# Performance work log

Hardware: AMD Instinct MI355X
Metric: run time of the kernel (lower is better)

## Reference

```python
import jax, jax.numpy as jnp
import numpy as np

N_NODES = 100000
N_EDGES = 1600000
FEAT = 128
EMB = 32
N_GRAPHS = 512


def gcn_conv(x, W, b, src, dst, deg_inv_sqrt):
    # PyG GCNConv: h = x @ W; propagate with norm = d_i^{-1/2} d_j^{-1/2} over A + I
    h = x @ W  # [N, out]
    norm = deg_inv_sqrt[src] * deg_inv_sqrt[dst]  # [E]
    msg = h[src] * norm[:, None]  # gather + scale
    agg = jax.ops.segment_sum(msg, dst, num_segments=N_NODES)
    # self-loop contribution: norm_ii = d_i^{-1}
    agg = agg + h * (deg_inv_sqrt * deg_inv_sqrt)[:, None]
    return agg + b


def setup_inputs() -> dict:
    key = jax.random.key(0)
    ks = jax.random.split(key, 10)
    x = jax.random.normal(ks[0], (N_NODES, FEAT), dtype=jnp.float32)
    edge_index = jax.random.randint(ks[1], (2, N_EDGES), 0, N_NODES, dtype=jnp.int64)
    batch_index = jnp.sort(jax.random.randint(ks[2], (N_NODES,), 0, N_GRAPHS, dtype=jnp.int64))
    # Glorot-ish init for weights (PyG GCNConv lin has no bias arg here but conv bias exists)
    def glorot(k, fan_in, fan_out):
        s = jnp.sqrt(6.0 / (fan_in + fan_out)).astype(jnp.float32)
        return jax.random.uniform(k, (fan_in, fan_out), jnp.float32, -s, s)
    W1 = glorot(ks[3], FEAT, EMB)
    b1 = jnp.zeros((EMB,), jnp.float32)
    W2 = glorot(ks[4], EMB, EMB)
    b2 = jnp.zeros((EMB,), jnp.float32)
    Wo = glorot(ks[5], EMB, 1)
    bo = jnp.zeros((1,), jnp.float32)
    return {"x": x, "edge_index": edge_index, "batch_index": batch_index,
            "W1": W1, "b1": b1, "W2": W2, "b2": b2, "Wo": Wo, "bo": bo}


def reference(x, edge_index, batch_index, W1, b1, W2, b2, Wo, bo):
    src, dst = edge_index[0], edge_index[1]
    # degree over A + I (edge weights = 1, counted on dst as in PyG)
    deg = jax.ops.segment_sum(jnp.ones((N_EDGES,), x.dtype), dst, num_segments=N_NODES) + 1.0
    deg_inv_sqrt = jax.lax.rsqrt(deg)

    out = jax.nn.relu(gcn_conv(x, W1, b1, src, dst, deg_inv_sqrt))
    out = jax.nn.relu(gcn_conv(out, W2, b2, src, dst, deg_inv_sqrt))

    # global mean pool over graphs
    summed = jax.ops.segment_sum(out, batch_index, num_segments=N_GRAPHS)  # [G, EMB]
    counts = jax.ops.segment_sum(jnp.ones((N_NODES,), x.dtype), batch_index, num_segments=N_GRAPHS)
    pooled = summed / jnp.maximum(counts, 1.0)[:, None]

    return pooled @ Wo + bo  # [G, 1]
```

## Files before the change

kernel.cpp:

```cpp
#include <hip/hip_runtime.h>
#include <hip/hip_fp16.h>

#define N_NODES 100000
#define N_EDGES 1600000
#define N_GRAPHS 512
#define FEAT 128
#define EMB 32
#define ZROW N_NODES
#define PADCAP (N_EDGES + 8 * N_NODES)
#define NCOPY 64
#define NBKT 250
#define NPB 400
#define ABLK 1024
#define EPB 1563
#define NTILE (N_NODES / 16)
#define AGB (N_NODES / 32)

typedef unsigned short u16;
typedef unsigned int u32;
typedef _Float16 f16;
typedef float f32x4 __attribute__((ext_vector_type(4)));
typedef unsigned short u16x4 __attribute__((ext_vector_type(4)));
typedef f16 f16x8 __attribute__((ext_vector_type(8)));

__device__ __forceinline__ int pad8(int d) { return (d + 7) & ~7; }

__device__ __forceinline__ float4 h4_to_f4(u16x4 v) {
  union { unsigned int u; __half2 h; } a, b;
  a.u = (unsigned int)v.x | ((unsigned int)v.y << 16);
  b.u = (unsigned int)v.z | ((unsigned int)v.w << 16);
  float2 f0 = __half22float2(a.h);
  float2 f1 = __half22float2(b.h);
  return make_float4(f0.x, f0.y, f1.x, f1.y);
}

__device__ __forceinline__ u16x4 f4_to_h4(float4 f) {
  union { unsigned int u; __half2 h; } a, b;
  a.h = __float22half2_rn(make_float2(f.x, f.y));
  b.h = __float22half2_rn(make_float2(f.z, f.w));
  u16x4 r;
  r.x = (u16)(a.u & 0xffff); r.y = (u16)(a.u >> 16);
  r.z = (u16)(b.u & 0xffff); r.w = (u16)(b.u >> 16);
  return r;
}


__global__ __launch_bounds__(256) void k_node_init(const int* __restrict__ degcnt,
                                                   float* __restrict__ dis,
                                                   u16* __restrict__ hs1) {
  int i = blockIdx.x * 256 + threadIdx.x;
  if (i < N_NODES) dis[i] = rsqrtf((float)degcnt[i] + 1.0f);
  if (i < EMB) hs1[(size_t)ZROW * EMB + i] = 0;
}

__global__ __launch_bounds__(512) void k_gcnt(const int* __restrict__ batch,
                                              int* __restrict__ gcnt) {
  __shared__ int first[N_GRAPHS + 1];
  int g = threadIdx.x;
  int lo = 0, hi = N_NODES;
  while (lo < hi) {
    int mid = (lo + hi) >> 1;
    if (batch[mid] < g) lo = mid + 1; else hi = mid;
  }
  first[g] = lo;
  if (g == 0) first[N_GRAPHS] = N_NODES;
  __syncthreads();
  gcnt[g] = first[g + 1] - first[g];
}


__global__ __launch_bounds__(256) void k_scanA(const int* __restrict__ degcnt,
                                               int* __restrict__ blocksum) {
  __shared__ int sh[256];
  int t = threadIdx.x;
  int base = blockIdx.x * 1024;
  int s = 0;
#pragma unroll
  for (int j = 0; j < 4; j++) {
    int idx = base + t * 4 + j;
    if (idx < N_NODES) s += pad8(degcnt[idx]);
  }
  sh[t] = s;
  __syncthreads();
  for (int off = 128; off > 0; off >>= 1) {
    if (t < off) sh[t] += sh[t + off];
    __syncthreads();
  }
  if (t == 0) blocksum[blockIdx.x] = sh[0];
}

__global__ __launch_bounds__(128) void k_scanB(const int* __restrict__ blocksum,
                                               int* __restrict__ blockoff,
                                               int* __restrict__ total_out, int nb) {
  __shared__ int sh[128];
  int t = threadIdx.x;
  int v = (t < nb) ? blocksum[t] : 0;
  sh[t] = v;
  __syncthreads();
  for (int off = 1; off < 128; off <<= 1) {
    int add = (t >= off) ? sh[t - off] : 0;
    __syncthreads();
    sh[t] += add;
    __syncthreads();
  }
  if (t < nb) blockoff[t] = sh[t] - v;
  if (t == nb - 1) total_out[0] = sh[t];
}

__global__ __launch_bounds__(256) void k_scanC(const int* __restrict__ degcnt,
                                               const int* __restrict__ blockoff,
                                               int* __restrict__ row_ptr) {
  __shared__ int sh[256];
  int t = threadIdx.x;
  int base = blockIdx.x * 1024;
  int v[4];
#pragma unroll
  for (int j = 0; j < 4; j++) {
    int idx = base + t * 4 + j;
    v[j] = (idx < N_NODES) ? pad8(degcnt[idx]) : 0;
  }
  int tsum = v[0] + v[1] + v[2] + v[3];
  sh[t] = tsum;
  __syncthreads();
  for (int off = 1; off < 256; off <<= 1) {
    int add = (t >= off) ? sh[t - off] : 0;
    __syncthreads();
    sh[t] += add;
    __syncthreads();
  }
  int p = sh[t] - tsum + blockoff[blockIdx.x];
#pragma unroll
  for (int j = 0; j < 4; j++) {
    int idx = base + t * 4 + j;
    if (idx < N_NODES) row_ptr[idx] = p;
    p += v[j];
  }
}


__global__ __launch_bounds__(256) void k_binA(const int* __restrict__ dst,
                                              int* __restrict__ cnt) {
  __shared__ int h[NBKT];
  int k = blockIdx.x, t = threadIdx.x;
  for (int i = t; i < NBKT; i += 256) h[i] = 0;
  __syncthreads();
  int e0 = k * EPB;
  int e1 = min(e0 + EPB, N_EDGES);
  for (int e = e0 + t; e < e1; e += 256)
    atomicAdd(&h[(u32)dst[e] / (u32)NPB], 1);
  __syncthreads();
  for (int i = t; i < NBKT; i += 256) cnt[k * NBKT + i] = h[i];
}

__global__ __launch_bounds__(256) void k_binscanA(const int* __restrict__ cnt,
                                                  int* __restrict__ off,
                                                  int* __restrict__ tot) {
  __shared__ int sh[256];
  int b = blockIdx.x, t = threadIdx.x;
  int v[4];
#pragma unroll
  for (int j = 0; j < 4; j++) v[j] = cnt[(t * 4 + j) * NBKT + b];
  int tsum = v[0] + v[1] + v[2] + v[3];
  sh[t] = tsum;
  __syncthreads();
  for (int o = 1; o < 256; o <<= 1) {
    int add = (t >= o) ? sh[t - o] : 0;
    __syncthreads();
    sh[t] += add;
    __syncthreads();
  }
  int p = sh[t] - tsum;
#pragma unroll
  for (int j = 0; j < 4; j++) {
    off[(t * 4 + j) * NBKT + b] = p;
    p += v[j];
  }
  if (t == 255) tot[b] = p;
}

__global__ __launch_bounds__(256) void k_binscanB(const int* __restrict__ tot,
                                                  int* __restrict__ base) {
  __shared__ int sh[256];
  int t = threadIdx.x;
  int v = (t < NBKT) ? tot[t] : 0;
  sh[t] = v;
  __syncthreads();
  for (int o = 1; o < 256; o <<= 1) {
    int add = (t >= o) ? sh[t - o] : 0;
    __syncthreads();
    sh[t] += add;
    __syncthreads();
  }
  if (t < NBKT) base[t] = sh[t] - v;
  if (t == NBKT - 1) base[NBKT] = sh[t];
}

__global__ __launch_bounds__(256) void k_binscat(const int* __restrict__ src,
                                                 const int* __restrict__ dst,
                                                 const int* __restrict__ off,
                                                 const int* __restrict__ base,
                                                 u32* __restrict__ binbuf) {
  __shared__ int posB[NBKT];
  __shared__ int h[NBKT];
  int k = blockIdx.x, t = threadIdx.x;
  for (int i = t; i < NBKT; i += 256) {
    posB[i] = base[i] + off[k * NBKT + i];
    h[i] = 0;
  }
  __syncthreads();
  int e0 = k * EPB;
  int e1 = min(e0 + EPB, N_EDGES);
  for (int e = e0 + t; e < e1; e += 256) {
    u32 d = (u32)dst[e];
    int b = d / (u32)NPB;
    int r = atomicAdd(&h[b], 1);
    binbuf[posB[b] + r] = (u32)src[e] * (u32)NPB + (d - (u32)b * NPB);
  }
}

__global__ __launch_bounds__(256) void k_bdeg(const u32* __restrict__ binbuf,
                                              const int* __restrict__ base,
                                              int* __restrict__ degcnt) {
  __shared__ int c[NPB];
  int b = blockIdx.x, t = threadIdx.x;
  for (int i = t; i < NPB; i += 256) c[i] = 0;
  __syncthreads();
  int s0 = base[b], s1 = base[b + 1];
  for (int i = s0 + t; i < s1; i += 256) {
    u32 p = binbuf[i];
    u32 s = p / (u32)NPB;
    atomicAdd(&c[p - s * (u32)NPB], 1);
  }
  __syncthreads();
  for (int i = t; i < NPB; i += 256) degcnt[b * NPB + i] = c[i];
}

__global__ __launch_bounds__(256) void k_fillB(const u32* __restrict__ binbuf,
                                               const int* __restrict__ base,
                                               const int* __restrict__ row_ptr,
                                               int* __restrict__ col) {
  __shared__ int rp[NPB + 1];
  __shared__ int cur[NPB];
  int b = blockIdx.x, t = threadIdx.x;
  for (int i = t; i < NPB + 1; i += 256) rp[i] = row_ptr[b * NPB + i];
  for (int i = t; i < NPB; i += 256) cur[i] = 0;
  __syncthreads();
  int s0 = base[b], s1 = base[b + 1];
  for (int i = s0 + t; i < s1; i += 256) {
    u32 p = binbuf[i];
    u32 s = p / (u32)NPB;
    int ld = p - s * (u32)NPB;
    int pos = atomicAdd(&cur[ld], 1);
    col[rp[ld] + pos] = (int)s;
  }
  __syncthreads();
  for (int ld = t; ld < NPB; ld += 256) {
    int bs = rp[ld], len = rp[ld + 1] - bs, c = cur[ld];
    for (int j = c; j < len; j++) col[bs + j] = ZROW;
  }
}


__global__ __launch_bounds__(256) void k_gemm1(const float* __restrict__ x,
                                               const float* __restrict__ W1,
                                               const float* __restrict__ dis,
                                               u16* __restrict__ hs1) {
  int wid = (blockIdx.x * 256 + threadIdx.x) >> 6;
  if (wid >= NTILE) return;
  int l = threadIdx.x & 63;
  int m = l & 15, q = l >> 4;
  f16x8 B[4][2];
#pragma unroll
  for (int s = 0; s < 4; ++s)
#pragma unroll
    for (int h = 0; h < 2; ++h)
#pragma unroll
      for (int j = 0; j < 8; ++j)
        B[s][h][j] = (f16)W1[(s * 32 + q * 8 + j) * EMB + h * 16 + m];
  int row = wid * 16 + m;
  const float* xr = x + (size_t)row * FEAT + q * 8;
  f32x4 acc0 = {0.f, 0.f, 0.f, 0.f}, acc1 = {0.f, 0.f, 0.f, 0.f};
#pragma unroll
  for (int s = 0; s < 4; ++s) {
    f32x4 xa = __builtin_nontemporal_load((const f32x4*)(xr + s * 32));
    f32x4 xb = __builtin_nontemporal_load((const f32x4*)(xr + s * 32 + 4));
    f16x8 A;
    A[0] = (f16)xa.x; A[1] = (f16)xa.y; A[2] = (f16)xa.z; A[3] = (f16)xa.w;
    A[4] = (f16)xb.x; A[5] = (f16)xb.y; A[6] = (f16)xb.z; A[7] = (f16)xb.w;
    acc0 = __builtin_amdgcn_mfma_f32_16x16x32_f16(A, B[s][0], acc0, 0, 0, 0);
    acc1 = __builtin_amdgcn_mfma_f32_16x16x32_f16(A, B[s][1], acc1, 0, 0, 0);
  }
  f32x4 dq = *(const f32x4*)(dis + wid * 16 + q * 4);
  u16* o = hs1 + (size_t)(wid * 16) * EMB;
#pragma unroll
  for (int i = 0; i < 4; ++i) {
    int r = q * 4 + i;
    float dv = (i == 0) ? dq.x : (i == 1) ? dq.y : (i == 2) ? dq.z : dq.w;
    o[(size_t)r * EMB + m]      = __half_as_ushort(__float2half_rn(acc0[i] * dv));
    o[(size_t)r * EMB + 16 + m] = __half_as_ushort(__float2half_rn(acc1[i] * dv));
  }
}

__global__ __launch_bounds__(256) void k_gemm2(const u16* __restrict__ in1,
                                               const float* __restrict__ W2,
                                               const float* __restrict__ dis,
                                               u16* __restrict__ hs2) {
  int wid = (blockIdx.x * 256 + threadIdx.x) >> 6;
  if (wid >= NTILE) return;
  int l = threadIdx.x & 63;
  int m = l & 15, q = l >> 4;
  f16x8 B[2];
#pragma unroll
  for (int h = 0; h < 2; ++h)
#pragma unroll
    for (int j = 0; j < 8; ++j)
      B[h][j] = (f16)W2[(q * 8 + j) * EMB + h * 16 + m];
  int row = wid * 16 + m;
  f16x8 A = *(const f16x8*)(in1 + (size_t)row * EMB + q * 8);
  f32x4 acc0 = {0.f, 0.f, 0.f, 0.f}, acc1 = {0.f, 0.f, 0.f, 0.f};
  acc0 = __builtin_amdgcn_mfma_f32_16x16x32_f16(A, B[0], acc0, 0, 0, 0);
  acc1 = __builtin_amdgcn_mfma_f32_16x16x32_f16(A, B[1], acc1, 0, 0, 0);
  f32x4 dq = *(const f32x4*)(dis + wid * 16 + q * 4);
  u16* o = hs2 + (size_t)(wid * 16) * EMB;
#pragma unroll
  for (int i = 0; i < 4; ++i) {
    int r = q * 4 + i;
    float dv = (i == 0) ? dq.x : (i == 1) ? dq.y : (i == 2) ? dq.z : dq.w;
    o[(size_t)r * EMB + m]      = __half_as_ushort(__float2half_rn(acc0[i] * dv));
    o[(size_t)r * EMB + 16 + m] = __half_as_ushort(__float2half_rn(acc1[i] * dv));
  }
}


__device__ __forceinline__ void acc4(float4& A, u16x4 v) {
  float4 f = h4_to_f4(v);
  A.x += f.x; A.y += f.y; A.z += f.z; A.w += f.w;
}

__device__ __forceinline__ float4 agg_node(const u16* __restrict__ hs,
                                           const int* __restrict__ row_ptr,
                                           const int* __restrict__ col,
                                           int node, int sub) {
  const u16x4* t4 = (const u16x4*)hs;
  int a0 = row_ptr[node];
  int na = row_ptr[node + 1] - a0;
  const int* cp = col + a0;
  int4 c0 = *(const int4*)cp;
  int4 c1 = *(const int4*)(cp + 4);
  float4 A = make_float4(0.f, 0.f, 0.f, 0.f);
  for (int i = 0; i < na; i += 8) {
    u16x4 v0 = t4[(size_t)c0.x * 8 + sub];
    u16x4 v1 = t4[(size_t)c0.y * 8 + sub];
    u16x4 v2 = t4[(size_t)c0.z * 8 + sub];
    u16x4 v3 = t4[(size_t)c0.w * 8 + sub];
    u16x4 v4 = t4[(size_t)c1.x * 8 + sub];
    u16x4 v5 = t4[(size_t)c1.y * 8 + sub];
    u16x4 v6 = t4[(size_t)c1.z * 8 + sub];
    u16x4 v7 = t4[(size_t)c1.w * 8 + sub];
    if (i + 8 < na) {
      c0 = *(const int4*)(cp + i + 8);
      c1 = *(const int4*)(cp + i + 12);
    }
    acc4(A, v0); acc4(A, v1); acc4(A, v2); acc4(A, v3);
    acc4(A, v4); acc4(A, v5); acc4(A, v6); acc4(A, v7);
  }
  acc4(A, t4[(size_t)node * 8 + sub]);
  return A;
}

__device__ __forceinline__ float4 relu_row(float4 acc, float d, float4 bq) {
  float4 o;
  o.x = fmaxf(fmaf(acc.x, d, bq.x), 0.f);
  o.y = fmaxf(fmaf(acc.y, d, bq.y), 0.f);
  o.z = fmaxf(fmaf(acc.z, d, bq.z), 0.f);
  o.w = fmaxf(fmaf(acc.w, d, bq.w), 0.f);
  return o;
}

__global__ __launch_bounds__(256) void k_agg1(const u16* __restrict__ hs,
                                              const int* __restrict__ row_ptr,
                                              const int* __restrict__ col,
                                              const float* __restrict__ dis,
                                              const float* __restrict__ b,
                                              u16* __restrict__ out) {
  int t = threadIdx.x;
  int l = t & 63;
  int node = blockIdx.x * 32 + (t >> 6) * 8 + (l >> 3);
  int sub = l & 7;
  float4 A = agg_node(hs, row_ptr, col, node, sub);
  float4 bq = ((const float4*)b)[sub];
  float4 o = relu_row(A, dis[node], bq);
  ((u16x4*)(out + (size_t)node * EMB))[sub] = f4_to_h4(o);
}

__global__ __launch_bounds__(256) void k_agg2pool(const u16* __restrict__ hs,
                                                  const int* __restrict__ row_ptr,
                                                  const int* __restrict__ col,
                                                  const float* __restrict__ dis,
                                                  const float* __restrict__ b2,
                                                  const float* __restrict__ Wo,
                                                  const int* __restrict__ batch,
                                                  float* __restrict__ gaccP) {
  int t = threadIdx.x;
  int l = t & 63;
  int node = blockIdx.x * 32 + (t >> 6) * 8 + (l >> 3);
  int sub = l & 7;
  float4 A = agg_node(hs, row_ptr, col, node, sub);
  float4 bq = ((const float4*)b2)[sub];
  float4 wq = ((const float4*)Wo)[sub];
  float4 o = relu_row(A, dis[node], bq);
  float p = o.x * wq.x + o.y * wq.y + o.z * wq.z + o.w * wq.w;
  p += __shfl_xor(p, 1);
  p += __shfl_xor(p, 2);
  p += __shfl_xor(p, 4);
  if (sub == 0)
    atomicAdd(&gaccP[(node & (NCOPY - 1)) * N_GRAPHS + batch[node]], p);
}

__global__ __launch_bounds__(256) void k_finalize(const float* __restrict__ gaccP,
                                                  const int* __restrict__ gcnt,
                                                  const float* __restrict__ bo,
                                                  float* __restrict__ out) {
  int g = blockIdx.x * 256 + threadIdx.x;
  if (g < N_GRAPHS) {
    float s = 0.f;
#pragma unroll 8
    for (int c = 0; c < NCOPY; ++c) s += gaccP[c * N_GRAPHS + g];
    out[g] = s / fmaxf((float)gcnt[g], 1.0f) + bo[0];
  }
}


extern "C" void kernel_launch(void* const* d_in, const int* in_sizes, int n_in,
                              void* d_out, int out_size, void* d_ws, size_t ws_size,
                              hipStream_t stream) {
  const float* x     = (const float*)d_in[0];
  const int*   ei    = (const int*)d_in[1];
  const int*   batch = (const int*)d_in[2];
  const float* W1    = (const float*)d_in[3];
  const float* b1    = (const float*)d_in[4];
  const float* W2    = (const float*)d_in[5];
  const float* b2    = (const float*)d_in[6];
  const float* Wo    = (const float*)d_in[7];
  const float* bo    = (const float*)d_in[8];
  float* out = (float*)d_out;

  const int* src = ei;
  const int* dst = ei + N_EDGES;

  char* w = (char*)d_ws;
  float* gaccP   = (float*)w;  w += (size_t)NCOPY * N_GRAPHS * 4;
  size_t zero_bytes = (size_t)(w - (char*)d_ws);
  int*   degcnt  = (int*)w;    w += (size_t)N_NODES * 4;
  int*   gcnt    = (int*)w;    w += (size_t)N_GRAPHS * 4;
  int*   row_ptr = (int*)w;    w += (size_t)(N_NODES + 4) * 4;
  int*   blocksum= (int*)w;    w += 128 * 4;
  int*   blockoff= (int*)w;    w += 128 * 4;
  int*   cnt     = (int*)w;    w += (size_t)ABLK * NBKT * 4;
  int*   boff    = (int*)w;    w += (size_t)ABLK * NBKT * 4;
  int*   btot    = (int*)w;    w += (size_t)(NBKT + 8) * 4;
  int*   bbase   = (int*)w;    w += (size_t)(NBKT + 8) * 4;
  int*   col     = (int*)w;    w += (size_t)PADCAP * 4;
  float* dis     = (float*)w;  w += (size_t)N_NODES * 4;
  u16*   hs1     = (u16*)w;    w += (size_t)(N_NODES + 1) * EMB * 2;
  u16*   out1    = (u16*)w;    w += (size_t)N_NODES * EMB * 2;
  u32*   binbuf  = (u32*)out1;
  u16*   hs2     = hs1;

  const int NB  = (N_NODES + 255) / 256;
  const int SB  = (N_NODES + 1023) / 1024;
  const int GB  = (NTILE * 64 + 255) / 256;

  (void)hipMemsetAsync(d_ws, 0, zero_bytes, stream);

  k_binA<<<ABLK, 256, 0, stream>>>(dst, cnt);
  k_binscanA<<<NBKT, 256, 0, stream>>>(cnt, boff, btot);
  k_binscanB<<<1, 256, 0, stream>>>(btot, bbase);
  k_binscat<<<ABLK, 256, 0, stream>>>(src, dst, boff, bbase, binbuf);
  k_bdeg<<<NBKT, 256, 0, stream>>>(binbuf, bbase, degcnt);

  k_node_init<<<NB, 256, 0, stream>>>(degcnt, dis, hs1);
  k_gcnt<<<1, 512, 0, stream>>>(batch, gcnt);
  k_scanA<<<SB, 256, 0, stream>>>(degcnt, blocksum);
  k_scanB<<<1, 128, 0, stream>>>(blocksum, blockoff, row_ptr + N_NODES, SB);
  k_scanC<<<SB, 256, 0, stream>>>(degcnt, blockoff, row_ptr);
  k_fillB<<<NBKT, 256, 0, stream>>>(binbuf, bbase, row_ptr, col);

  k_gemm1<<<GB, 256, 0, stream>>>(x, W1, dis, hs1);
  k_agg1<<<AGB, 256, 0, stream>>>(hs1, row_ptr, col, dis, b1, out1);
  k_gemm2<<<GB, 256, 0, stream>>>(out1, W2, dis, hs2);
  k_agg2pool<<<AGB, 256, 0, stream>>>(hs2, row_ptr, col, dis, b2, Wo, batch, gaccP);
  k_finalize<<<2, 256, 0, stream>>>(gaccP, gcnt, bo, out);
}
```

Measured before the change: 247.1 us.

## Drop CSR build; aggregate directly from dst-binned edge buffer via LDS atomics

Removes the CSR construction (degree scan kernels, fill kernel, padded col array) and instead aggregates neighbor features straight from the dst-bucketed edge buffer. Each block owns a 100-node bucket and accumulates messages into a shared-memory float accumulator with LDS atomics, then applies self-loop, normalization, bias and ReLU. Degree and rsqrt are fused into one kernel, and bucket counts and block sizes are retuned. This saves several launches and the col write and read, at the cost of LDS atomic contention and unordered float summation.

```diff
diff --git a/kernel.cpp b/kernel.cpp
--- a/kernel.cpp
+++ b/kernel.cpp
@@ -7,14 +7,14 @@
 #define FEAT 128
 #define EMB 32
 #define ZROW N_NODES
-#define PADCAP (N_EDGES + 8 * N_NODES)
 #define NCOPY 64
-#define NBKT 250
-#define NPB 400
-#define ABLK 1024
-#define EPB 1563
+#define NBKT 1000
+#define NPB 100
+#define LDSW 33
+#define ABLK 512
+#define EPB 3125
 #define NTILE (N_NODES / 16)
-#define AGB (N_NODES / 32)
+#define SENT ((u32)ZROW * (u32)NPB)
 
 typedef unsigned short u16;
 typedef unsigned int u32;
@@ -22,8 +22,6 @@
 typedef float f32x4 __attribute__((ext_vector_type(4)));
 typedef unsigned short u16x4 __attribute__((ext_vector_type(4)));
 typedef f16 f16x8 __attribute__((ext_vector_type(8)));
-
-__device__ __forceinline__ int pad8(int d) { return (d + 7) & ~7; }
 
 __device__ __forceinline__ float4 h4_to_f4(u16x4 v) {
   union { unsigned int u; __half2 h; } a, b;
@@ -44,14 +42,15 @@
   return r;
 }
 
-
-__global__ __launch_bounds__(256) void k_node_init(const int* __restrict__ degcnt,
-                                                   float* __restrict__ dis,
-                                                   u16* __restrict__ hs1) {
-  int i = blockIdx.x * 256 + threadIdx.x;
-  if (i < N_NODES) dis[i] = rsqrtf((float)degcnt[i] + 1.0f);
-  if (i < EMB) hs1[(size_t)ZROW * EMB + i] = 0;
-}
+__device__ __forceinline__ float4 relu_row(float4 acc, float d, float4 bq) {
+  float4 o;
+  o.x = fmaxf(fmaf(acc.x, d, bq.x), 0.f);
+  o.y = fmaxf(fmaf(acc.y, d, bq.y), 0.f);
+  o.z = fmaxf(fmaf(acc.z, d, bq.z), 0.f);
+  o.w = fmaxf(fmaf(acc.w, d, bq.w), 0.f);
+  return o;
+}
+
 
 __global__ __launch_bounds__(512) void k_gcnt(const int* __restrict__ batch,
                                               int* __restrict__ gcnt) {
@@ -69,75 +68,6 @@
 }
 
 
-__global__ __launch_bounds__(256) void k_scanA(const int* __restrict__ degcnt,
-                                               int* __restrict__ blocksum) {
-  __shared__ int sh[256];
-  int t = threadIdx.x;
-  int base = blockIdx.x * 1024;
-  int s = 0;
-#pragma unroll
-  for (int j = 0; j < 4; j++) {
-    int idx = base + t * 4 + j;
-    if (idx < N_NODES) s += pad8(degcnt[idx]);
-  }
-  sh[t] = s;
-  __syncthreads();
-  for (int off = 128; off > 0; off >>= 1) {
-    if (t < off) sh[t] += sh[t + off];
-    __syncthreads();
-  }
-  if (t == 0) blocksum[blockIdx.x] = sh[0];
-}
-
-__global__ __launch_bounds__(128) void k_scanB(const int* __restrict__ blocksum,
-                                               int* __restrict__ blockoff,
-                                               int* __restrict__ total_out, int nb) {
-  __shared__ int sh[128];
-  int t = threadIdx.x;
-  int v = (t < nb) ? blocksum[t] : 0;
-  sh[t] = v;
-  __syncthreads();
-  for (int off = 1; off < 128; off <<= 1) {
-    int add = (t >= off) ? sh[t - off] : 0;
-    __syncthreads();
-    sh[t] += add;
-    __syncthreads();
-  }
-  if (t < nb) blockoff[t] = sh[t] - v;
-  if (t == nb - 1) total_out[0] = sh[t];
-}
-
-__global__ __launch_bounds__(256) void k_scanC(const int* __restrict__ degcnt,
-                                               const int* __restrict__ blockoff,
-                                               int* __restrict__ row_ptr) {
-  __shared__ int sh[256];
-  int t = threadIdx.x;
-  int base = blockIdx.x * 1024;
-  int v[4];
-#pragma unroll
-  for (int j = 0; j < 4; j++) {
-    int idx = base + t * 4 + j;
-    v[j] = (idx < N_NODES) ? pad8(degcnt[idx]) : 0;
-  }
-  int tsum = v[0] + v[1] + v[2] + v[3];
-  sh[t] = tsum;
-  __syncthreads();
-  for (int off = 1; off < 256; off <<= 1) {
-    int add = (t >= off) ? sh[t - off] : 0;
-    __syncthreads();
-    sh[t] += add;
-    __syncthreads();
-  }
-  int p = sh[t] - tsum + blockoff[blockIdx.x];
-#pragma unroll
-  for (int j = 0; j < 4; j++) {
-    int idx = base + t * 4 + j;
-    if (idx < N_NODES) row_ptr[idx] = p;
-    p += v[j];
-  }
-}
-
-
 __global__ __launch_bounds__(256) void k_binA(const int* __restrict__ dst,
                                               int* __restrict__ cnt) {
   __shared__ int h[NBKT];
@@ -157,10 +87,10 @@
                                                   int* __restrict__ tot) {
   __shared__ int sh[256];
   int b = blockIdx.x, t = threadIdx.x;
-  int v[4];
-#pragma unroll
-  for (int j = 0; j < 4; j++) v[j] = cnt[(t * 4 + j) * NBKT + b];
-  int tsum = v[0] + v[1] + v[2] + v[3];
+  int v[2];
+#pragma unroll
+  for (int j = 0; j < 2; j++) v[j] = cnt[(t * 2 + j) * NBKT + b];
+  int tsum = v[0] + v[1];
   sh[t] = tsum;
   __syncthreads();
   for (int o = 1; o < 256; o <<= 1) {
@@ -171,8 +101,8 @@
   }
   int p = sh[t] - tsum;
 #pragma unroll
-  for (int j = 0; j < 4; j++) {
-    off[(t * 4 + j) * NBKT + b] = p;
+  for (int j = 0; j < 2; j++) {
+    off[(t * 2 + j) * NBKT + b] = p;
     p += v[j];
   }
   if (t == 255) tot[b] = p;
@@ -182,8 +112,14 @@
                                                   int* __restrict__ base) {
   __shared__ int sh[256];
   int t = threadIdx.x;
-  int v = (t < NBKT) ? tot[t] : 0;
-  sh[t] = v;
+  int v[4];
+#pragma unroll
+  for (int j = 0; j < 4; j++) {
+    int i = t * 4 + j;
+    v[j] = (i < NBKT) ? tot[i] : 0;
+  }
+  int tsum = v[0] + v[1] + v[2] + v[3];
+  sh[t] = tsum;
   __syncthreads();
   for (int o = 1; o < 256; o <<= 1) {
     int add = (t >= o) ? sh[t - o] : 0;
@@ -191,8 +127,14 @@
     sh[t] += add;
     __syncthreads();
   }
-  if (t < NBKT) base[t] = sh[t] - v;
-  if (t == NBKT - 1) base[NBKT] = sh[t];
+  int p = sh[t] - tsum;
+#pragma unroll
+  for (int j = 0; j < 4; j++) {
+    int i = t * 4 + j;
+    if (i < NBKT) base[i] = p;
+    p += v[j];
+  }
+  if (t == 255) base[NBKT] = p;
 }
 
 __global__ __launch_bounds__(256) void k_binscat(const int* __restrict__ src,
@@ -218,46 +160,25 @@
   }
 }
 
-__global__ __launch_bounds__(256) void k_bdeg(const u32* __restrict__ binbuf,
-                                              const int* __restrict__ base,
-                                              int* __restrict__ degcnt) {
+__global__ __launch_bounds__(256) void k_deg_dis(const u32* __restrict__ binbuf,
+                                                 const int* __restrict__ base,
+                                                 float* __restrict__ dis,
+                                                 u16* __restrict__ hs1) {
   __shared__ int c[NPB];
   int b = blockIdx.x, t = threadIdx.x;
   for (int i = t; i < NPB; i += 256) c[i] = 0;
   __syncthreads();
   int s0 = base[b], s1 = base[b + 1];
   for (int i = s0 + t; i < s1; i += 256) {
-    u32 p = binbuf[i];
+    u32 p = __builtin_nontemporal_load(&binbuf[i]);
     u32 s = p / (u32)NPB;
     atomicAdd(&c[p - s * (u32)NPB], 1);
   }
   __syncthreads();
-  for (int i = t; i < NPB; i += 256) degcnt[b * NPB + i] = c[i];
-}
-
-__global__ __launch_bounds__(256) void k_fillB(const u32* __restrict__ binbuf,
-                                               const int* __restrict__ base,
-                                               const int* __restrict__ row_ptr,
-                                               int* __restrict__ col) {
-  __shared__ int rp[NPB + 1];
-  __shared__ int cur[NPB];
-  int b = blockIdx.x, t = threadIdx.x;
-  for (int i = t; i < NPB + 1; i += 256) rp[i] = row_ptr[b * NPB + i];
-  for (int i = t; i < NPB; i += 256) cur[i] = 0;
-  __syncthreads();
-  int s0 = base[b], s1 = base[b + 1];
-  for (int i = s0 + t; i < s1; i += 256) {
-    u32 p = binbuf[i];
-    u32 s = p / (u32)NPB;
-    int ld = p - s * (u32)NPB;
-    int pos = atomicAdd(&cur[ld], 1);
-    col[rp[ld] + pos] = (int)s;
-  }
-  __syncthreads();
-  for (int ld = t; ld < NPB; ld += 256) {
-    int bs = rp[ld], len = rp[ld + 1] - bs, c = cur[ld];
-    for (int j = c; j < len; j++) col[bs + j] = ZROW;
-  }
+  for (int i = t; i < NPB; i += 256)
+    dis[b * NPB + i] = rsqrtf((float)c[i] + 1.0f);
+  if (b == 0)
+    for (int i = t; i < EMB; i += 256) hs1[(size_t)ZROW * EMB + i] = 0;
 }
 
 
@@ -332,89 +253,96 @@
 }
 
 
-__device__ __forceinline__ void acc4(float4& A, u16x4 v) {
-  float4 f = h4_to_f4(v);
-  A.x += f.x; A.y += f.y; A.z += f.z; A.w += f.w;
-}
-
-__device__ __forceinline__ float4 agg_node(const u16* __restrict__ hs,
-                                           const int* __restrict__ row_ptr,
-                                           const int* __restrict__ col,
-                                           int node, int sub) {
-  const u16x4* t4 = (const u16x4*)hs;
-  int a0 = row_ptr[node];
-  int na = row_ptr[node + 1] - a0;
-  const int* cp = col + a0;
-  int4 c0 = *(const int4*)cp;
-  int4 c1 = *(const int4*)(cp + 4);
-  float4 A = make_float4(0.f, 0.f, 0.f, 0.f);
-  for (int i = 0; i < na; i += 8) {
-    u16x4 v0 = t4[(size_t)c0.x * 8 + sub];
-    u16x4 v1 = t4[(size_t)c0.y * 8 + sub];
-    u16x4 v2 = t4[(size_t)c0.z * 8 + sub];
-    u16x4 v3 = t4[(size_t)c0.w * 8 + sub];
-    u16x4 v4 = t4[(size_t)c1.x * 8 + sub];
-    u16x4 v5 = t4[(size_t)c1.y * 8 + sub];
-    u16x4 v6 = t4[(size_t)c1.z * 8 + sub];
-    u16x4 v7 = t4[(size_t)c1.w * 8 + sub];
-    if (i + 8 < na) {
-      c0 = *(const int4*)(cp + i + 8);
-      c1 = *(const int4*)(cp + i + 12);
-    }
-    acc4(A, v0); acc4(A, v1); acc4(A, v2); acc4(A, v3);
-    acc4(A, v4); acc4(A, v5); acc4(A, v6); acc4(A, v7);
-  }
-  acc4(A, t4[(size_t)node * 8 + sub]);
-  return A;
-}
-
-__device__ __forceinline__ float4 relu_row(float4 acc, float d, float4 bq) {
-  float4 o;
-  o.x = fmaxf(fmaf(acc.x, d, bq.x), 0.f);
-  o.y = fmaxf(fmaf(acc.y, d, bq.y), 0.f);
-  o.z = fmaxf(fmaf(acc.z, d, bq.z), 0.f);
-  o.w = fmaxf(fmaf(acc.w, d, bq.w), 0.f);
-  return o;
+__device__ __forceinline__ void agg_edges(float (*acc)[LDSW],
+                                          const u16x4* __restrict__ t4,
+                                          const u32* __restrict__ binbuf,
+                                          int eb, int ee, int G, int sub) {
+  for (int e = eb + G; e < ee; e += 128) {
+    u32 p0 = __builtin_nontemporal_load(&binbuf[e]);
+    u32 p1 = (e + 32 < ee) ? __builtin_nontemporal_load(&binbuf[e + 32]) : SENT;
+    u32 p2 = (e + 64 < ee) ? __builtin_nontemporal_load(&binbuf[e + 64]) : SENT;
+    u32 p3 = (e + 96 < ee) ? __builtin_nontemporal_load(&binbuf[e + 96]) : SENT;
+    u32 q0 = p0 / (u32)NPB; int l0 = (int)(p0 - q0 * NPB);
+    u32 q1 = p1 / (u32)NPB; int l1 = (int)(p1 - q1 * NPB);
+    u32 q2 = p2 / (u32)NPB; int l2 = (int)(p2 - q2 * NPB);
+    u32 q3 = p3 / (u32)NPB; int l3 = (int)(p3 - q3 * NPB);
+    u16x4 v0 = t4[(size_t)q0 * 8 + sub];
+    u16x4 v1 = t4[(size_t)q1 * 8 + sub];
+    u16x4 v2 = t4[(size_t)q2 * 8 + sub];
+    u16x4 v3 = t4[(size_t)q3 * 8 + sub];
+    float4 f0 = h4_to_f4(v0), f1 = h4_to_f4(v1);
+    float4 f2 = h4_to_f4(v2), f3 = h4_to_f4(v3);
+    float* a0 = &acc[l0][sub * 4];
+    float* a1 = &acc[l1][sub * 4];
+    float* a2 = &acc[l2][sub * 4];
+    float* a3 = &acc[l3][sub * 4];
+    atomicAdd(a0 + 0, f0.x); atomicAdd(a0 + 1, f0.y);
+    atomicAdd(a0 + 2, f0.z); atomicAdd(a0 + 3, f0.w);
+    atomicAdd(a1 + 0, f1.x); atomicAdd(a1 + 1, f1.y);
+    atomicAdd(a1 + 2, f1.z); atomicAdd(a1 + 3, f1.w);
+    atomicAdd(a2 + 0, f2.x); atomicAdd(a2 + 1, f2.y);
+    atomicAdd(a2 + 2, f2.z); atomicAdd(a2 + 3, f2.w);
+    atomicAdd(a3 + 0, f3.x); atomicAdd(a3 + 1, f3.y);
+    atomicAdd(a3 + 2, f3.z); atomicAdd(a3 + 3, f3.w);
+  }
 }
 
 __global__ __launch_bounds__(256) void k_agg1(const u16* __restrict__ hs,
-                                              const int* __restrict__ row_ptr,
-                                              const int* __restrict__ col,
+                                              const u32* __restrict__ binbuf,
+                                              const int* __restrict__ base,
                                               const float* __restrict__ dis,
                                               const float* __restrict__ b,
                                               u16* __restrict__ out) {
-  int t = threadIdx.x;
-  int l = t & 63;
-  int node = blockIdx.x * 32 + (t >> 6) * 8 + (l >> 3);
-  int sub = l & 7;
-  float4 A = agg_node(hs, row_ptr, col, node, sub);
-  float4 bq = ((const float4*)b)[sub];
-  float4 o = relu_row(A, dis[node], bq);
-  ((u16x4*)(out + (size_t)node * EMB))[sub] = f4_to_h4(o);
+  __shared__ float acc[NPB][LDSW];
+  int t = threadIdx.x, bkt = blockIdx.x;
+  for (int i = t; i < NPB * LDSW; i += 256) ((float*)acc)[i] = 0.f;
+  __syncthreads();
+  const u16x4* t4 = (const u16x4*)hs;
+  agg_edges(acc, t4, binbuf, base[bkt], base[bkt + 1], t >> 3, t & 7);
+  __syncthreads();
+  for (int idx = t; idx < NPB * 8; idx += 256) {
+    int ld = idx >> 3, sb = idx & 7;
+    int node = bkt * NPB + ld;
+    float4 sv = h4_to_f4(t4[(size_t)node * 8 + sb]);
+    const float* ap = &acc[ld][sb * 4];
+    float4 A = make_float4(ap[0] + sv.x, ap[1] + sv.y, ap[2] + sv.z, ap[3] + sv.w);
+    float4 bq = ((const float4*)b)[sb];
+    float4 o = relu_row(A, dis[node], bq);
+    ((u16x4*)(out + (size_t)node * EMB))[sb] = f4_to_h4(o);
+  }
 }
 
 __global__ __launch_bounds__(256) void k_agg2pool(const u16* __restrict__ hs,
-                                                  const int* __restrict__ row_ptr,
-                                                  const int* __restrict__ col,
+                                                  const u32* __restrict__ binbuf,
+                                                  const int* __restrict__ base,
                                                   const float* __restrict__ dis,
                                                   const float* __restrict__ b2,
                                                   const float* __restrict__ Wo,
                                                   const int* __restrict__ batch,
                                                   float* __restrict__ gaccP) {
-  int t = threadIdx.x;
-  int l = t & 63;
-  int node = blockIdx.x * 32 + (t >> 6) * 8 + (l >> 3);
-  int sub = l & 7;
-  float4 A = agg_node(hs, row_ptr, col, node, sub);
-  float4 bq = ((const float4*)b2)[sub];
-  float4 wq = ((const float4*)Wo)[sub];
-  float4 o = relu_row(A, dis[node], bq);
-  float p = o.x * wq.x + o.y * wq.y + o.z * wq.z + o.w * wq.w;
-  p += __shfl_xor(p, 1);
-  p += __shfl_xor(p, 2);
-  p += __shfl_xor(p, 4);
-  if (sub == 0)
-    atomicAdd(&gaccP[(node & (NCOPY - 1)) * N_GRAPHS + batch[node]], p);
+  __shared__ float acc[NPB][LDSW];
+  int t = threadIdx.x, bkt = blockIdx.x;
+  for (int i = t; i < NPB * LDSW; i += 256) ((float*)acc)[i] = 0.f;
+  __syncthreads();
+  const u16x4* t4 = (const u16x4*)hs;
+  agg_edges(acc, t4, binbuf, base[bkt], base[bkt + 1], t >> 3, t & 7);
+  __syncthreads();
+  for (int idx = t; idx < NPB * 8; idx += 256) {
+    int ld = idx >> 3, sb = idx & 7;
+    int node = bkt * NPB + ld;
+    float4 sv = h4_to_f4(t4[(size_t)node * 8 + sb]);
+    const float* ap = &acc[ld][sb * 4];
+    float4 A = make_float4(ap[0] + sv.x, ap[1] + sv.y, ap[2] + sv.z, ap[3] + sv.w);
+    float4 bq = ((const float4*)b2)[sb];
+    float4 wq = ((const float4*)Wo)[sb];
+    float4 o = relu_row(A, dis[node], bq);
+    float p = o.x * wq.x + o.y * wq.y + o.z * wq.z + o.w * wq.w;
+    p += __shfl_xor(p, 1);
+    p += __shfl_xor(p, 2);
+    p += __shfl_xor(p, 4);
+    if (sb == 0)
+      atomicAdd(&gaccP[(node & (NCOPY - 1)) * N_GRAPHS + batch[node]], p);
+  }
 }
 
 __global__ __launch_bounds__(256) void k_finalize(const float* __restrict__ gaccP,
@@ -451,25 +379,18 @@
   char* w = (char*)d_ws;
   float* gaccP   = (float*)w;  w += (size_t)NCOPY * N_GRAPHS * 4;
   size_t zero_bytes = (size_t)(w - (char*)d_ws);
-  int*   degcnt  = (int*)w;    w += (size_t)N_NODES * 4;
   int*   gcnt    = (int*)w;    w += (size_t)N_GRAPHS * 4;
-  int*   row_ptr = (int*)w;    w += (size_t)(N_NODES + 4) * 4;
-  int*   blocksum= (int*)w;    w += 128 * 4;
-  int*   blockoff= (int*)w;    w += 128 * 4;
   int*   cnt     = (int*)w;    w += (size_t)ABLK * NBKT * 4;
   int*   boff    = (int*)w;    w += (size_t)ABLK * NBKT * 4;
   int*   btot    = (int*)w;    w += (size_t)(NBKT + 8) * 4;
   int*   bbase   = (int*)w;    w += (size_t)(NBKT + 8) * 4;
-  int*   col     = (int*)w;    w += (size_t)PADCAP * 4;
+  u32*   binbuf  = (u32*)w;    w += (size_t)N_EDGES * 4;
   float* dis     = (float*)w;  w += (size_t)N_NODES * 4;
   u16*   hs1     = (u16*)w;    w += (size_t)(N_NODES + 1) * EMB * 2;
   u16*   out1    = (u16*)w;    w += (size_t)N_NODES * EMB * 2;
-  u32*   binbuf  = (u32*)out1;
   u16*   hs2     = hs1;
 
-  const int NB  = (N_NODES + 255) / 256;
-  const int SB  = (N_NODES + 1023) / 1024;
-  const int GB  = (NTILE * 64 + 255) / 256;
+  const int GB = (NTILE * 64 + 255) / 256;
 
   (void)hipMemsetAsync(d_ws, 0, zero_bytes, stream);
 
@@ -477,18 +398,12 @@
   k_binscanA<<<NBKT, 256, 0, stream>>>(cnt, boff, btot);
   k_binscanB<<<1, 256, 0, stream>>>(btot, bbase);
   k_binscat<<<ABLK, 256, 0, stream>>>(src, dst, boff, bbase, binbuf);
-  k_bdeg<<<NBKT, 256, 0, stream>>>(binbuf, bbase, degcnt);
-
-  k_node_init<<<NB, 256, 0, stream>>>(degcnt, dis, hs1);
+  k_deg_dis<<<NBKT, 256, 0, stream>>>(binbuf, bbase, dis, hs1);
   k_gcnt<<<1, 512, 0, stream>>>(batch, gcnt);
-  k_scanA<<<SB, 256, 0, stream>>>(degcnt, blocksum);
-  k_scanB<<<1, 128, 0, stream>>>(blocksum, blockoff, row_ptr + N_NODES, SB);
-  k_scanC<<<SB, 256, 0, stream>>>(degcnt, blockoff, row_ptr);
-  k_fillB<<<NBKT, 256, 0, stream>>>(binbuf, bbase, row_ptr, col);
 
   k_gemm1<<<GB, 256, 0, stream>>>(x, W1, dis, hs1);
-  k_agg1<<<AGB, 256, 0, stream>>>(hs1, row_ptr, col, dis, b1, out1);
+  k_agg1<<<NBKT, 256, 0, stream>>>(hs1, binbuf, bbase, dis, b1, out1);
   k_gemm2<<<GB, 256, 0, stream>>>(out1, W2, dis, hs2);
-  k_agg2pool<<<AGB, 256, 0, stream>>>(hs2, row_ptr, col, dis, b2, Wo, batch, gaccP);
+  k_agg2pool<<<NBKT, 256, 0, stream>>>(hs2, binbuf, bbase, dis, b2, Wo, batch, gaccP);
   k_finalize<<<2, 256, 0, stream>>>(gaccP, gcnt, bo, out);
 }
```

New measurement: 744.5 us. 3.01x slower.
